# Kernel tuning notes

Measured on AMD Instinct MI355X. Metric: run time of the kernel, lower is better.

The kernel has to match this reference:

```python
import jax, jax.numpy as jnp
import numpy as np

DIM = 1024
N_HEAD = 16
HEAD_DIM = DIM // N_HEAD
B, T = 4, 2048


def setup_inputs() -> dict:
    key = jax.random.key(0)
    k1, k2, k3 = jax.random.split(key, 3)
    x = jax.random.normal(k1, (B, T, DIM), dtype=jnp.float32)
    attn_mask = jnp.ones((B, T), dtype=bool)
    # nn.Linear(dim, dim*3, bias=False): weight [3*dim, dim]; store transposed [dim, 3*dim]
    w_qkv = jax.random.normal(k2, (DIM, 3 * DIM), dtype=jnp.float32) * (DIM ** -0.5)
    w_out = jax.random.normal(k3, (DIM, DIM), dtype=jnp.float32) * (DIM ** -0.5)
    return {"x": x, "w_qkv": w_qkv, "w_out": w_out, "attn_mask": attn_mask}


def reference(x, w_qkv, w_out, attn_mask):
    b, t, c = x.shape
    qkv = (x @ w_qkv).reshape(b, t, 3, N_HEAD, HEAD_DIM)
    qkv = jnp.transpose(qkv, (2, 0, 3, 1, 4))  # [3, B, H, T, D]
    q, k, v = qkv[0], qkv[1], qkv[2]
    scale = HEAD_DIM ** -0.5
    scores = jnp.einsum('bhtd,bhsd->bhts', q, k) * scale  # [B, H, T, T]
    causal = jnp.tril(jnp.ones((t, t), dtype=bool))        # True where attend allowed
    keep = causal[None, None, :, :] & attn_mask[:, None, None, :]
    scores = jnp.where(keep, scores, -jnp.inf)
    probs = jax.nn.softmax(scores, axis=-1)
    out = jnp.einsum('bhts,bhsd->bhtd', probs, v)          # [B, H, T, D]
    out = jnp.transpose(out, (0, 2, 1, 3)).reshape(b, t, c)
    return out @ w_out
```

## Files before the change

### kernel.cpp

```cpp
#include <hip/hip_runtime.h>

#define DIMN 1024
#define NH   16
#define HD   64
#define BB   4
#define TT   2048
#define MTOK (BB*TT)
#define N3   (3*DIMN)

typedef unsigned short u16;
typedef u16   u16x4  __attribute__((ext_vector_type(4)));
typedef __bf16 bf16x8 __attribute__((ext_vector_type(8)));
typedef float float4v __attribute__((ext_vector_type(4)));
typedef _Float16 f16;
typedef f16 f16x2 __attribute__((ext_vector_type(2)));
typedef f16 f16x4 __attribute__((ext_vector_type(4)));
typedef f16 f16x8 __attribute__((ext_vector_type(8)));

#if __has_builtin(__builtin_amdgcn_exp2f)
#define EXP2(x) __builtin_amdgcn_exp2f(x)
#else
#define EXP2(x) exp2f(x)
#endif

__device__ __forceinline__ u16 f2bf(float f) {
  union { float f; unsigned u; } v; v.f = f;
  unsigned u = v.u;
  return (u16)((u + 0x7FFFu + ((u >> 16) & 1u)) >> 16);
}
__device__ __forceinline__ u16 f2h(float f) {
  union { f16 h; u16 u; } v; v.h = (f16)f; return v.u;
}

__device__ __forceinline__ void gld_lds16(const void* g, void* l) {
  __builtin_amdgcn_global_load_lds(
      (const __attribute__((address_space(1))) void*)g,
      (__attribute__((address_space(3))) void*)l, 16, 0, 0);
}

__device__ __forceinline__ float4v mfma16bf(bf16x8 a, bf16x8 b, float4v c) {
  return __builtin_amdgcn_mfma_f32_16x16x32_bf16(a, b, c, 0, 0, 0);
}
__device__ __forceinline__ float4v mfma32h(f16x8 a, f16x8 b, float4v c) {
  return __builtin_amdgcn_mfma_f32_16x16x32_f16(a, b, c, 0, 0, 0);
}

#define PREP_CVT   (MTOK*DIMN/1024)
#define PREP_TQKV  (N3/32 * DIMN/32)
#define PREP_TOUT  (DIMN/32 * DIMN/32)
__global__ __launch_bounds__(256) void k_prep(
    const float* __restrict__ x, u16* __restrict__ xb,
    const float* __restrict__ w_qkv, u16* __restrict__ wqkvT,
    const float* __restrict__ w_out, u16* __restrict__ woutT)
{
  __shared__ float tile[32][33];
  const int bid = blockIdx.x, tid = threadIdx.x;
  if (bid < PREP_CVT) {
    int i = (bid * 256 + tid) * 4;
    float4v v = *(const float4v*)(x + i);
    u16x4 o;
    o[0] = f2bf(v[0]); o[1] = f2bf(v[1]); o[2] = f2bf(v[2]); o[3] = f2bf(v[3]);
    *(u16x4*)(xb + i) = o;
    return;
  }
  const float* w; u16* wT; int N, t;
  if (bid < PREP_CVT + PREP_TQKV) { t = bid - PREP_CVT; w = w_qkv; wT = wqkvT; N = N3; }
  else { t = bid - PREP_CVT - PREP_TQKV; w = w_out; wT = woutT; N = DIMN; }
  const int K = DIMN;
  int n0 = (t % (N/32)) * 32, k0 = (t / (N/32)) * 32;
  int tx = tid & 31, ty = tid >> 5;
#pragma unroll
  for (int i = 0; i < 4; ++i)
    tile[ty + i*8][tx] = w[(k0 + ty + i*8)*N + n0 + tx];
  __syncthreads();
#pragma unroll
  for (int i = 0; i < 4; ++i)
    wT[(n0 + ty + i*8)*K + k0 + tx] = f2bf(tile[tx][ty + i*8]);
}

__global__ __launch_bounds__(256) void k_gemm_qkv(
    const u16* __restrict__ xb, const u16* __restrict__ wT,
    u16* __restrict__ qb, u16* __restrict__ kb, u16* __restrict__ vb2)
{
  __shared__ __align__(16) u16 As[128*64];
  __shared__ __align__(16) u16 Bs[128*64];
  const int m0 = blockIdx.x * 128, n0 = blockIdx.y * 128;
  const int tid = threadIdx.x;
  const int lane = tid & 63, wv = tid >> 6;
  const int quad = lane >> 4, l16 = lane & 15;
  const int wm = (wv >> 1) * 64, wn = (wv & 1) * 64;

  const char* gA[4]; const char* gB[4]; int lofs[4];
#pragma unroll
  for (int l = 0; l < 4; ++l) {
    int c = l*256 + tid;
    int row = c >> 3, pos = c & 7;
    int ps = pos ^ (row & 7);
    gA[l] = (const char*)xb + (size_t)(m0 + row)*2048 + (size_t)(ps*16);
    gB[l] = (const char*)wT + (size_t)(n0 + row)*2048 + (size_t)(ps*16);
    lofs[l] = c*16;
  }

  int aOff[4][2], bOff[4][2];
#pragma unroll
  for (int kh = 0; kh < 2; ++kh) {
    int px = ((kh*4 + quad) ^ (l16 & 7)) * 16;
#pragma unroll
    for (int mt = 0; mt < 4; ++mt) {
      aOff[mt][kh] = (wm + mt*16 + l16)*128 + px;
      bOff[mt][kh] = (wn + mt*16 + l16)*128 + px;
    }
  }

  float4v acc[4][4] = {};

  for (int kt = 0; kt < DIMN; kt += 64) {
#pragma unroll
    for (int l = 0; l < 4; ++l) gld_lds16(gA[l] + kt*2, (char*)As + lofs[l]);
#pragma unroll
    for (int l = 0; l < 4; ++l) gld_lds16(gB[l] + kt*2, (char*)Bs + lofs[l]);
    __syncthreads();
    bf16x8 af[4][2], bfv[4][2];
#pragma unroll
    for (int mt = 0; mt < 4; ++mt) {
      af[mt][0]  = *(const bf16x8*)((const char*)As + aOff[mt][0]);
      af[mt][1]  = *(const bf16x8*)((const char*)As + aOff[mt][1]);
      bfv[mt][0] = *(const bf16x8*)((const char*)Bs + bOff[mt][0]);
      bfv[mt][1] = *(const bf16x8*)((const char*)Bs + bOff[mt][1]);
    }
#pragma unroll
    for (int mt = 0; mt < 4; ++mt)
#pragma unroll
      for (int nt = 0; nt < 4; ++nt) {
        acc[mt][nt] = mfma16bf(af[mt][0], bfv[nt][0], acc[mt][nt]);
        acc[mt][nt] = mfma16bf(af[mt][1], bfv[nt][1], acc[mt][nt]);
      }
    __syncthreads();
  }

  const float QSCALE = 0.125f * 1.4426950408889634f;
#pragma unroll
  for (int mt = 0; mt < 4; ++mt)
#pragma unroll
    for (int nt = 0; nt < 4; ++nt) {
      int col = n0 + wn + nt*16 + l16;
      int which = col >> 10, cc = col & 1023, h = cc >> 6, d = cc & 63;
      int row0 = m0 + wm + mt*16 + quad*4;
      int b = row0 >> 11, t0 = row0 & (TT-1);
      int bh = b*NH + h;
      if (which == 2) {
        u16x4 pk;
#pragma unroll
        for (int r = 0; r < 4; ++r) pk[r] = f2h(acc[mt][nt][r]);
        *(u16x4*)(vb2 + (bh*HD + d)*TT + t0) = pk;
      } else {
        u16* dst = (which == 0) ? qb : kb;
        float s = (which == 0) ? QSCALE : 1.0f;
#pragma unroll
        for (int r = 0; r < 4; ++r)
          dst[(bh*TT + t0 + r)*HD + d] = f2h(acc[mt][nt][r] * s);
      }
    }
}

__global__ __launch_bounds__(256) void k_attn(
    const u16* __restrict__ qb, const u16* __restrict__ kb,
    const u16* __restrict__ vb2, u16* __restrict__ ab)
{
  __shared__ __align__(16) u16 Ks0[64*64];
  __shared__ __align__(16) u16 Ks1[64*64];
  __shared__ __align__(16) u16 Vt0[64*64];
  __shared__ __align__(16) u16 Vt1[64*64];
  const int id = (int)blockIdx.x;
  const int xcd = id & 7, slot = id >> 3;
  const int bh = xcd * 8 + (slot & 7);
  const int jA = slot >> 3;
  const int b = bh >> 4, h = bh & 15;
  const int qg0 = jA * 64;
  const int qg1 = (31 - jA) * 64;
  const int tid = threadIdx.x, lane = tid & 63, wv = tid >> 6;
  const int quad = lane >> 4, l16 = lane & 15;
  const u16* Qb = qb + bh * (TT*HD);
  const u16* Kb = kb + bh * (TT*HD);
  const u16* Vb = vb2 + bh * (HD*TT);

  f16x8 bq[2][2];
  {
    int qr0 = qg0 + wv*16 + l16;
    bq[0][0] = *(const f16x8*)(Qb + qr0*HD + quad*8);
    bq[0][1] = *(const f16x8*)(Qb + qr0*HD + 32 + quad*8);
    int qr1 = qg1 + wv*16 + l16;
    bq[1][0] = *(const f16x8*)(Qb + qr1*HD + quad*8);
    bq[1][1] = *(const f16x8*)(Qb + qr1*HD + 32 + quad*8);
  }

  float4v o[2][4] = {};
  float4v ol[2] = {};

  int kof0[4], kof1[4], vof[4][4];
#pragma unroll
  for (int st = 0; st < 4; ++st) {
    int srow = st*16 + l16, sw = srow & 7;
    kof0[st] = srow*128 + ((quad ^ sw) * 16);
    kof1[st] = srow*128 + (((4 + quad) ^ sw) * 16);
#pragma unroll
    for (int dt = 0; dt < 4; ++dt) {
      int vrow = dt*16 + l16, vsw = vrow & 7;
      int chunk = st*2 + (quad >> 1);
      vof[st][dt] = vrow*128 + ((chunk ^ vsw) * 16) + (quad & 1) * 8;
    }
  }

  const int cA = tid, cB = tid + 256;
  const int rowA = cA >> 3, posA = cA & 7, rowB = cB >> 3, posB = cB & 7;
  const int gA = posA ^ (rowA & 7), gB = posB ^ (rowB & 7);

  const int nt = (qg1 >> 6) + 1;
  const f16x8 ones8 = {(f16)1.f, (f16)1.f, (f16)1.f, (f16)1.f,
                       (f16)1.f, (f16)1.f, (f16)1.f, (f16)1.f};
  const int ql = wv*16 + l16;

#define PREFETCH(s1, Kd, Vd) do {                                   \
    gld_lds16(Kb + ((s1)+rowA)*HD + gA*8, (char*)(Kd) + cA*16);     \
    gld_lds16(Kb + ((s1)+rowB)*HD + gB*8, (char*)(Kd) + cB*16);     \
    gld_lds16(Vb + rowA*TT + (s1) + gA*8, (char*)(Vd) + cA*16);     \
    gld_lds16(Vb + rowB*TT + (s1) + gB*8, (char*)(Vd) + cB*16);     \
  } while (0)

#define TILE_BODY(K_, V_, i) do {                                           \
    const bool g0a = ((i) <= jA);                                           \
    float4v sc[2][4];                                                       \
    __builtin_amdgcn_s_setprio(1);                                          \
    _Pragma("unroll")                                                       \
    for (int st = 0; st < 4; ++st) {                                        \
      f16x8 ak0 = *(const f16x8*)((const char*)(K_) + kof0[st]);            \
      f16x8 ak1 = *(const f16x8*)((const char*)(K_) + kof1[st]);            \
      if (g0a) {                                                            \
        float4v s = {};                                                     \
        s = mfma32h(ak0, bq[0][0], s);                                      \
        s = mfma32h(ak1, bq[0][1], s);                                      \
        sc[0][st] = s;                                                      \
      }                                                                     \
      float4v s = {};                                                       \
      s = mfma32h(ak0, bq[1][0], s);                                        \
      s = mfma32h(ak1, bq[1][1], s);                                        \
      sc[1][st] = s;                                                        \
    }                                                                       \
    __builtin_amdgcn_s_setprio(0);                                          \
    if ((i) == jA) {                                                        \
      _Pragma("unroll")                                                     \
      for (int st = 0; st < 4; ++st)                                        \
        _Pragma("unroll")                                                   \
        for (int r = 0; r < 4; ++r)                                         \
          if (st*16 + quad*4 + r > ql) sc[0][st][r] = -1e30f;               \
    }                                                                       \
    if ((i) == nt - 1) {                                                    \
      _Pragma("unroll")                                                     \
      for (int st = 0; st < 4; ++st)                                        \
        _Pragma("unroll")                                                   \
        for (int r = 0; r < 4; ++r)                                         \
          if (st*16 + quad*4 + r > ql) sc[1][st][r] = -1e30f;               \
    }                                                                       \
    f16x8 ap8[2][2];                                                        \
    _Pragma("unroll")                                                       \
    for (int g = 0; g < 2; ++g) {                                           \
      if (g == 0 && !g0a) continue;                                         \
      _Pragma("unroll")                                                     \
      for (int sp = 0; sp < 2; ++sp) {                                      \
        float p0 = EXP2(sc[g][2*sp][0]);                                    \
        float p1 = EXP2(sc[g][2*sp][1]);                                    \
        float p2 = EXP2(sc[g][2*sp][2]);                                    \
        float p3 = EXP2(sc[g][2*sp][3]);                                    \
        float p4 = EXP2(sc[g][2*sp+1][0]);                                  \
        float p5 = EXP2(sc[g][2*sp+1][1]);                                  \
        float p6 = EXP2(sc[g][2*sp+1][2]);                                  \
        float p7 = EXP2(sc[g][2*sp+1][3]);                                  \
        f16x2 a01 = __builtin_bit_cast(f16x2, __builtin_amdgcn_cvt_pkrtz(p0, p1)); \
        f16x2 a23 = __builtin_bit_cast(f16x2, __builtin_amdgcn_cvt_pkrtz(p2, p3)); \
        f16x2 a45 = __builtin_bit_cast(f16x2, __builtin_amdgcn_cvt_pkrtz(p4, p5)); \
        f16x2 a67 = __builtin_bit_cast(f16x2, __builtin_amdgcn_cvt_pkrtz(p6, p7)); \
        f16x4 alo = __builtin_shufflevector(a01, a23, 0, 1, 2, 3);          \
        f16x4 ahi = __builtin_shufflevector(a45, a67, 0, 1, 2, 3);          \
        ap8[g][sp] = __builtin_shufflevector(alo, ahi, 0,1,2,3,4,5,6,7);    \
      }                                                                     \
      ol[g] = mfma32h(ap8[g][0], ones8, ol[g]);                             \
      ol[g] = mfma32h(ap8[g][1], ones8, ol[g]);                             \
    }                                                                       \
    __builtin_amdgcn_s_setprio(1);                                          \
    _Pragma("unroll")                                                       \
    for (int sp = 0; sp < 2; ++sp)                                          \
      _Pragma("unroll")                                                     \
      for (int dt = 0; dt < 4; ++dt) {                                      \
        f16x4 bl = *(const f16x4*)((const char*)(V_) + vof[2*sp][dt]);      \
        f16x4 bh2 = *(const f16x4*)((const char*)(V_) + vof[2*sp+1][dt]);   \
        f16x8 bv8 = __builtin_shufflevector(bl, bh2, 0,1,2,3,4,5,6,7);      \
        if (g0a) o[0][dt] = mfma32h(ap8[0][sp], bv8, o[0][dt]);             \
        o[1][dt] = mfma32h(ap8[1][sp], bv8, o[1][dt]);                      \
      }                                                                     \
    __builtin_amdgcn_s_setprio(0);                                          \
  } while (0)

  PREFETCH(0, Ks0, Vt0);

  for (int ii = 0; ii < nt; ii += 2) {
    __syncthreads();
    if (ii + 1 < nt) PREFETCH((ii+1)*64, Ks1, Vt1);
    TILE_BODY(Ks0, Vt0, ii);
    if (ii + 1 < nt) {
      __syncthreads();
      if (ii + 2 < nt) PREFETCH((ii+2)*64, Ks0, Vt0);
      TILE_BODY(Ks1, Vt1, ii+1);
    }
  }
#undef TILE_BODY
#undef PREFETCH

#pragma unroll
  for (int g = 0; g < 2; ++g) {
    int qg = g ? qg1 : qg0;
#pragma unroll
    for (int r = 0; r < 4; ++r) {
      float inv_r = 1.0f / ol[g][r];
      int t = qg + wv*16 + quad*4 + r;
#pragma unroll
      for (int dt = 0; dt < 4; ++dt)
        ab[(b*TT + t)*DIMN + h*HD + dt*16 + l16] = f2bf(o[g][dt][r] * inv_r);
    }
  }
}

__global__ __launch_bounds__(256) void k_gemm_out(
    const u16* __restrict__ ab, const u16* __restrict__ wT, float* __restrict__ out)
{
  __shared__ __align__(16) u16 As[128*64];
  __shared__ __align__(16) u16 Bs[128*64];
  const int m0 = blockIdx.x * 128, n0 = blockIdx.y * 128;
  const int tid = threadIdx.x;
  const int lane = tid & 63, wv = tid >> 6;
  const int quad = lane >> 4, l16 = lane & 15;
  const int wm = (wv >> 1) * 64, wn = (wv & 1) * 64;

  const char* gA[4]; const char* gB[4]; int lofs[4];
#pragma unroll
  for (int l = 0; l < 4; ++l) {
    int c = l*256 + tid;
    int row = c >> 3, pos = c & 7;
    int ps = pos ^ (row & 7);
    gA[l] = (const char*)ab + (size_t)(m0 + row)*2048 + (size_t)(ps*16);
    gB[l] = (const char*)wT + (size_t)(n0 + row)*2048 + (size_t)(ps*16);
    lofs[l] = c*16;
  }

  int aOff[4][2], bOff[4][2];
#pragma unroll
  for (int kh = 0; kh < 2; ++kh) {
    int px = ((kh*4 + quad) ^ (l16 & 7)) * 16;
#pragma unroll
    for (int mt = 0; mt < 4; ++mt) {
      aOff[mt][kh] = (wm + mt*16 + l16)*128 + px;
      bOff[mt][kh] = (wn + mt*16 + l16)*128 + px;
    }
  }

  float4v acc[4][4] = {};

  for (int kt = 0; kt < DIMN; kt += 64) {
#pragma unroll
    for (int l = 0; l < 4; ++l) gld_lds16(gA[l] + kt*2, (char*)As + lofs[l]);
#pragma unroll
    for (int l = 0; l < 4; ++l) gld_lds16(gB[l] + kt*2, (char*)Bs + lofs[l]);
    __syncthreads();
    bf16x8 af[4][2], bfv[4][2];
#pragma unroll
    for (int mt = 0; mt < 4; ++mt) {
      af[mt][0]  = *(const bf16x8*)((const char*)As + aOff[mt][0]);
      af[mt][1]  = *(const bf16x8*)((const char*)As + aOff[mt][1]);
      bfv[mt][0] = *(const bf16x8*)((const char*)Bs + bOff[mt][0]);
      bfv[mt][1] = *(const bf16x8*)((const char*)Bs + bOff[mt][1]);
    }
#pragma unroll
    for (int mt = 0; mt < 4; ++mt)
#pragma unroll
      for (int nt = 0; nt < 4; ++nt) {
        acc[mt][nt] = mfma16bf(af[mt][0], bfv[nt][0], acc[mt][nt]);
        acc[mt][nt] = mfma16bf(af[mt][1], bfv[nt][1], acc[mt][nt]);
      }
    __syncthreads();
  }
#pragma unroll
  for (int mt = 0; mt < 4; ++mt)
#pragma unroll
    for (int nt = 0; nt < 4; ++nt) {
      int col = n0 + wn + nt*16 + l16;
#pragma unroll
      for (int r = 0; r < 4; ++r) {
        int row = m0 + wm + mt*16 + quad*4 + r;
        out[row*DIMN + col] = acc[mt][nt][r];
      }
    }
}

extern "C" void kernel_launch(void* const* d_in, const int* in_sizes, int n_in,
                              void* d_out, int out_size, void* d_ws, size_t ws_size,
                              hipStream_t stream) {
  const float* x     = (const float*)d_in[0];
  const float* w_qkv = (const float*)d_in[1];
  const float* w_out = (const float*)d_in[2];
  float* out = (float*)d_out;
  char* ws = (char*)d_ws;
  u16* xb    = (u16*)(ws);
  u16* wqkvT = (u16*)(ws + (16u << 20));
  u16* woutT = (u16*)(ws + (22u << 20));
  u16* qbuf  = (u16*)(ws + (24u << 20));
  u16* kbuf  = (u16*)(ws + (40u << 20));
  u16* vbuf  = (u16*)(ws + (56u << 20));
  u16* abuf  = xb;

  k_prep<<<dim3(PREP_CVT + PREP_TQKV + PREP_TOUT), 256, 0, stream>>>(
      x, xb, w_qkv, wqkvT, w_out, woutT);
  k_gemm_qkv<<<dim3(MTOK/128, N3/128), 256, 0, stream>>>(xb, wqkvT, qbuf, kbuf, vbuf);
  k_attn<<<dim3(16 * BB * NH), 256, 0, stream>>>(qbuf, kbuf, vbuf, abuf);
  k_gemm_out<<<dim3(MTOK/128, DIMN/128), 256, 0, stream>>>(abuf, woutT, out);
}
```

Measured before the change: 238.8 us.

## Shrink QKV GEMM K-tile to 32 and drop LDS swizzle

Changes the QKV projection GEMM to stage 32-wide K slices instead of 64-wide, halving LDS usage per block and removing the XOR swizzle on shared-memory addressing. This simplifies the address math and may allow higher occupancy. In exchange it doubles the number of loop iterations and barriers, and the unswizzled row layout can cause LDS bank conflicts on the fragment reads.

Result: no change. 243.5 us (+2.0%).

```diff
diff --git a/kernel.cpp b/kernel.cpp
--- a/kernel.cpp
+++ b/kernel.cpp
@@ -82,59 +82,41 @@
     const u16* __restrict__ xb, const u16* __restrict__ wT,
     u16* __restrict__ qb, u16* __restrict__ kb, u16* __restrict__ vb2)
 {
-  __shared__ __align__(16) u16 As[128*64];
-  __shared__ __align__(16) u16 Bs[128*64];
+  __shared__ __align__(16) u16 As[128*32];
+  __shared__ __align__(16) u16 Bs[128*32];
   const int m0 = blockIdx.x * 128, n0 = blockIdx.y * 128;
   const int tid = threadIdx.x;
   const int lane = tid & 63, wv = tid >> 6;
   const int quad = lane >> 4, l16 = lane & 15;
   const int wm = (wv >> 1) * 64, wn = (wv & 1) * 64;
-
-  const char* gA[4]; const char* gB[4]; int lofs[4];
-#pragma unroll
-  for (int l = 0; l < 4; ++l) {
-    int c = l*256 + tid;
-    int row = c >> 3, pos = c & 7;
-    int ps = pos ^ (row & 7);
-    gA[l] = (const char*)xb + (size_t)(m0 + row)*2048 + (size_t)(ps*16);
-    gB[l] = (const char*)wT + (size_t)(n0 + row)*2048 + (size_t)(ps*16);
-    lofs[l] = c*16;
-  }
-
-  int aOff[4][2], bOff[4][2];
-#pragma unroll
-  for (int kh = 0; kh < 2; ++kh) {
-    int px = ((kh*4 + quad) ^ (l16 & 7)) * 16;
-#pragma unroll
-    for (int mt = 0; mt < 4; ++mt) {
-      aOff[mt][kh] = (wm + mt*16 + l16)*128 + px;
-      bOff[mt][kh] = (wn + mt*16 + l16)*128 + px;
-    }
-  }
+  const int c0 = tid, c1 = tid + 256;
+  const u16* ga0 = xb + (m0 + (c0 >> 2)) * DIMN + (c0 & 3) * 8;
+  const u16* ga1 = xb + (m0 + (c1 >> 2)) * DIMN + (c1 & 3) * 8;
+  const u16* gb0 = wT + (n0 + (c0 >> 2)) * DIMN + (c0 & 3) * 8;
+  const u16* gb1 = wT + (n0 + (c1 >> 2)) * DIMN + (c1 & 3) * 8;
+  char* la0 = (char*)As + c0 * 16; char* la1 = (char*)As + c1 * 16;
+  char* lb0 = (char*)Bs + c0 * 16; char* lb1 = (char*)Bs + c1 * 16;
 
   float4v acc[4][4] = {};
 
-  for (int kt = 0; kt < DIMN; kt += 64) {
-#pragma unroll
-    for (int l = 0; l < 4; ++l) gld_lds16(gA[l] + kt*2, (char*)As + lofs[l]);
-#pragma unroll
-    for (int l = 0; l < 4; ++l) gld_lds16(gB[l] + kt*2, (char*)Bs + lofs[l]);
+  for (int kt = 0; kt < DIMN; kt += 32) {
+    gld_lds16(ga0 + kt, la0);
+    gld_lds16(ga1 + kt, la1);
+    gld_lds16(gb0 + kt, lb0);
+    gld_lds16(gb1 + kt, lb1);
     __syncthreads();
-    bf16x8 af[4][2], bfv[4][2];
-#pragma unroll
-    for (int mt = 0; mt < 4; ++mt) {
-      af[mt][0]  = *(const bf16x8*)((const char*)As + aOff[mt][0]);
-      af[mt][1]  = *(const bf16x8*)((const char*)As + aOff[mt][1]);
-      bfv[mt][0] = *(const bf16x8*)((const char*)Bs + bOff[mt][0]);
-      bfv[mt][1] = *(const bf16x8*)((const char*)Bs + bOff[mt][1]);
-    }
+    bf16x8 af[4], bfv[4];
 #pragma unroll
     for (int mt = 0; mt < 4; ++mt)
-#pragma unroll
-      for (int nt = 0; nt < 4; ++nt) {
-        acc[mt][nt] = mfma16bf(af[mt][0], bfv[nt][0], acc[mt][nt]);
-        acc[mt][nt] = mfma16bf(af[mt][1], bfv[nt][1], acc[mt][nt]);
-      }
+      af[mt] = *(const bf16x8*)&As[(wm + mt*16 + l16)*32 + quad*8];
+#pragma unroll
+    for (int nt = 0; nt < 4; ++nt)
+      bfv[nt] = *(const bf16x8*)&Bs[(wn + nt*16 + l16)*32 + quad*8];
+#pragma unroll
+    for (int mt = 0; mt < 4; ++mt)
+#pragma unroll
+      for (int nt = 0; nt < 4; ++nt)
+        acc[mt][nt] = mfma16bf(af[mt], bfv[nt], acc[mt][nt]);
     __syncthreads();
   }
 
```
